# Kernel optimization log

Measured on AMD Instinct MI355X. Metric: run time of the kernel, lower is better.

The kernel has to match this reference:

```python
import jax, jax.numpy as jnp
import numpy as np

N_HEADS = 16

def setup_inputs() -> dict:
    key = jax.random.key(0)
    k1, k2, k3 = jax.random.split(key, 3)
    B, L, D = 2, 2048, 1024
    x = jax.random.normal(k1, (B, L, D), dtype=jnp.float32)
    w_qkv = jax.random.normal(k2, (D, 3 * D), dtype=jnp.float32) * (D ** -0.5)
    w_proj = jax.random.normal(k3, (D, D), dtype=jnp.float32) * (D ** -0.5)
    return {"x": x, "w_qkv": w_qkv, "w_proj": w_proj}

def reference(x, w_qkv, w_proj):
    B, L, D = x.shape
    H = N_HEADS
    dh = D // H
    qkv = x @ w_qkv  # [B,L,3D]
    q, k, v = jnp.split(qkv, 3, axis=-1)
    def heads(t):
        return t.reshape(B, L, H, dh).transpose(0, 2, 1, 3)  # [B,H,L,dh]
    q, k, v = heads(q), heads(k), heads(v)
    s = jnp.einsum('bhqd,bhkd->bhqk', q, k) / jnp.sqrt(jnp.float32(dh))
    causal = jnp.tril(jnp.ones((L, L), dtype=bool))
    s = jnp.where(causal[None, None], s, jnp.float32(-jnp.inf))
    w = jax.nn.softmax(s, axis=-1)
    o = jnp.einsum('bhqk,bhkd->bhqd', w, v)  # [B,H,L,dh]
    o = o.transpose(0, 2, 1, 3).reshape(B, L, D)
    return o @ w_proj
```

## Files before the change

### kernel.cpp

```cpp
#include <hip/hip_runtime.h>
#include <hip/hip_bf16.h>
#include <cstddef>

typedef __attribute__((ext_vector_type(8))) short bf16x8;
typedef __attribute__((ext_vector_type(4))) float f32x4;
typedef __attribute__((ext_vector_type(4))) unsigned short us4;
typedef __attribute__((ext_vector_type(8))) unsigned short us8;
typedef unsigned short u16;
typedef unsigned int u32;

__device__ __forceinline__ u16 f2bf(float f) {
    unsigned u = __builtin_bit_cast(unsigned, f);
    u += 0x7FFFu + ((u >> 16) & 1u);
    return (u16)(u >> 16);
}
__device__ __forceinline__ float bf2f(u16 h) {
    unsigned u = ((unsigned)h) << 16;
    return __builtin_bit_cast(float, u);
}

__device__ __forceinline__ void gl_lds16(const u16* g, u16* l) {
    __builtin_amdgcn_global_load_lds(
        (const __attribute__((address_space(1))) u32*)g,
        (__attribute__((address_space(3))) u32*)l, 16, 0, 0);
}

__device__ __forceinline__ bf16x8 ldswz(const u16* base, int row, int ck) {
    const u16* p = base + row * 64 + ((ck ^ (row & 7)) << 3);
    return __builtin_bit_cast(bf16x8, *(const us8*)p);
}

__global__ __launch_bounds__(256) void split_rm(const float* __restrict__ in,
                                                u16* __restrict__ hi,
                                                u16* __restrict__ lo, int n4) {
    int i = blockIdx.x * 256 + threadIdx.x;
    const int stride = gridDim.x * 256;
    for (; i < n4; i += stride) {
        f32x4 v = ((const f32x4*)in)[i];
        us4 h, l;
#pragma unroll
        for (int e = 0; e < 4; ++e) {
            u16 hb = f2bf(v[e]);
            h[e] = hb;
            l[e] = f2bf(v[e] - bf2f(hb));
        }
        ((us4*)hi)[i] = h;
        ((us4*)lo)[i] = l;
    }
}

__global__ __launch_bounds__(256) void split_T(const float* __restrict__ in, int inRS,
                                               u16* __restrict__ oh,
                                               u16* __restrict__ ol, int outRS) {
    __shared__ u16 Th[64][68], Tl[64][68];
    const int tid = threadIdx.x;
    const int sr = tid >> 4;
    const int sc = (tid & 15) * 4;
    const size_t r0 = (size_t)blockIdx.y * 64;
    const size_t c0 = (size_t)blockIdx.x * 64;

#pragma unroll
    for (int i = 0; i < 4; ++i) {
        int r = sr + i * 16;
        f32x4 v = *(const f32x4*)(in + (r0 + r) * inRS + c0 + sc);
#pragma unroll
        for (int e = 0; e < 4; ++e) {
            u16 hb = f2bf(v[e]);
            Th[sc + e][r] = hb;
            Tl[sc + e][r] = f2bf(v[e] - bf2f(hb));
        }
    }
    __syncthreads();
#pragma unroll
    for (int i = 0; i < 4; ++i) {
        int r = sr + i * 16;
        *(us4*)&oh[(c0 + r) * outRS + r0 + sc] = *(const us4*)&Th[r][sc];
        *(us4*)&ol[(c0 + r) * outRS + r0 + sc] = *(const us4*)&Tl[r][sc];
    }
}

__global__ __launch_bounds__(256) void gemm_bf(
    const u16* __restrict__ Ah_g, const u16* __restrict__ Al_g,
    const u16* __restrict__ Bh_g, const u16* __restrict__ Bl_g,
    int N, int K, int gy, int mode,
    float* __restrict__ Cf,
    u16* __restrict__ qsh, u16* __restrict__ qsl,
    u16* __restrict__ ksh, u16* __restrict__ ksl,
    float* __restrict__ vtmp) {
    __shared__ u16 Ah[128][40], Al[128][40];
    __shared__ u16 Bh[128][40], Bl[128][40];

    const int tid = threadIdx.x;
    const int nwg = gridDim.x;
    const int swz = (blockIdx.x & 7) * (nwg >> 3) + (blockIdx.x >> 3);
    const int bm = (swz % gy) * 128;
    const int bn = (swz / gy) * 128;

    const int arow0 = tid >> 3;
    const int akc   = (tid & 7) * 4;

    const u16* pAh = Ah_g + (size_t)(bm + arow0) * K + akc;
    const u16* pAl = Al_g + (size_t)(bm + arow0) * K + akc;
    const u16* pBh = Bh_g + (size_t)(bn + arow0) * K + akc;
    const u16* pBl = Bl_g + (size_t)(bn + arow0) * K + akc;

    us4 rah[4], ral[4], rbh[4], rbl[4];
#pragma unroll
    for (int c = 0; c < 4; ++c) {
        const size_t o = (size_t)(32 * c) * K;
        rah[c] = *(const us4*)(pAh + o);
        ral[c] = *(const us4*)(pAl + o);
        rbh[c] = *(const us4*)(pBh + o);
        rbl[c] = *(const us4*)(pBl + o);
    }

    const int lane = tid & 63;
    const int w    = tid >> 6;
    const int wm   = (w >> 1) * 64;
    const int wn   = (w & 1) * 64;
    const int lr   = lane & 15;
    const int lg   = lane >> 4;
    const int kb   = lg * 8;

    f32x4 acc[4][4] = {};

    const int NK = K >> 5;
    for (int kt = 0; kt < NK; ++kt) {
#pragma unroll
        for (int c = 0; c < 4; ++c) {
            const int row = arow0 + c * 32;
            *(us4*)&Ah[row][akc] = rah[c];
            *(us4*)&Al[row][akc] = ral[c];
            *(us4*)&Bh[row][akc] = rbh[c];
            *(us4*)&Bl[row][akc] = rbl[c];
        }
        __syncthreads();

        if (kt + 1 < NK) {
            pAh += 32; pAl += 32; pBh += 32; pBl += 32;
#pragma unroll
            for (int c = 0; c < 4; ++c) {
                const size_t o = (size_t)(32 * c) * K;
                rah[c] = *(const us4*)(pAh + o);
                ral[c] = *(const us4*)(pAl + o);
                rbh[c] = *(const us4*)(pBh + o);
                rbl[c] = *(const us4*)(pBl + o);
            }
        }

        bf16x8 fah[4], fal[4], fbh[4], fbl[4];
#pragma unroll
        for (int m = 0; m < 4; ++m) {
            fah[m] = __builtin_bit_cast(bf16x8, *(const us8*)&Ah[wm + m * 16 + lr][kb]);
            fal[m] = __builtin_bit_cast(bf16x8, *(const us8*)&Al[wm + m * 16 + lr][kb]);
        }
#pragma unroll
        for (int n = 0; n < 4; ++n) {
            fbh[n] = __builtin_bit_cast(bf16x8, *(const us8*)&Bh[wn + n * 16 + lr][kb]);
            fbl[n] = __builtin_bit_cast(bf16x8, *(const us8*)&Bl[wn + n * 16 + lr][kb]);
        }
#pragma unroll
        for (int m = 0; m < 4; ++m)
#pragma unroll
            for (int n = 0; n < 4; ++n) {
                acc[m][n] = __builtin_amdgcn_mfma_f32_16x16x32_bf16(fah[m], fbh[n], acc[m][n], 0, 0, 0);
                acc[m][n] = __builtin_amdgcn_mfma_f32_16x16x32_bf16(fah[m], fbl[n], acc[m][n], 0, 0, 0);
                acc[m][n] = __builtin_amdgcn_mfma_f32_16x16x32_bf16(fal[m], fbh[n], acc[m][n], 0, 0, 0);
            }
        __syncthreads();
    }

    const int orow = bm + wm + lg * 4;
    if (mode == 0) {
        const int ocol = bn + wn + lr;
#pragma unroll
        for (int m = 0; m < 4; ++m)
#pragma unroll
            for (int r = 0; r < 4; ++r) {
                const size_t row = (size_t)(orow + m * 16 + r);
#pragma unroll
                for (int n = 0; n < 4; ++n)
                    Cf[row * N + ocol + n * 16] = acc[m][n][r];
            }
    } else {
        const int sec = bn >> 10;
        const int cbase = (bn & 1023) + wn + lr;
#pragma unroll
        for (int m = 0; m < 4; ++m)
#pragma unroll
            for (int r = 0; r < 4; ++r) {
                const size_t row = (size_t)(orow + m * 16 + r);
#pragma unroll
                for (int n = 0; n < 4; ++n) {
                    float v = acc[m][n][r];
                    const size_t idx = row * 1024 + cbase + n * 16;
                    if (sec == 0) {
                        v *= 0.125f;
                        u16 hb = f2bf(v);
                        qsh[idx] = hb;
                        qsl[idx] = f2bf(v - bf2f(hb));
                    } else if (sec == 1) {
                        u16 hb = f2bf(v);
                        ksh[idx] = hb;
                        ksl[idx] = f2bf(v - bf2f(hb));
                    } else {
                        vtmp[idx] = v;
                    }
                }
            }
    }
}

__global__ __launch_bounds__(512, 4) void attn_v2(
    const u16* __restrict__ qsh, const u16* __restrict__ qsl,
    const u16* __restrict__ ksh, const u16* __restrict__ ksl,
    const u16* __restrict__ vth, const u16* __restrict__ vtl,
    u16* __restrict__ oh, u16* __restrict__ ol) {
    __shared__ u16 KH[4096], KL[4096], VH[4096], VL[4096];
    __shared__ u16 Ph[128][72], Pl[128][72];

    const int tid  = threadIdx.x;
    const int lane = tid & 63;
    const int w    = tid >> 6;
    const int wq0  = w * 16;
    const int lr   = lane & 15;
    const int lg   = lane >> 4;

    const int bid  = blockIdx.x;
    const int half = bid >> 8;
    const int idx  = bid & 255;
    const int bh   = idx & 31;
    const int jj   = idx >> 5;
    const int qt   = half ? jj : (15 - jj);
    const int b    = bh >> 4;
    const int h    = bh & 15;
    const int NT   = 2 * qt + 2;
    const size_t tokb = (size_t)b * 2048;

    const size_t qtok = tokb + (size_t)qt * 128 + wq0 + lr;
    const u16* qph = qsh + qtok * 1024 + h * 64 + lg * 8;
    const u16* qpl = qsl + qtok * 1024 + h * 64 + lg * 8;
    bf16x8 aqh[2], aql[2];
    aqh[0] = __builtin_bit_cast(bf16x8, *(const us8*)qph);
    aqh[1] = __builtin_bit_cast(bf16x8, *(const us8*)(qph + 32));
    aql[0] = __builtin_bit_cast(bf16x8, *(const us8*)qpl);
    aql[1] = __builtin_bit_cast(bf16x8, *(const us8*)(qpl + 32));

    const int rl    = lane >> 3;
    const int rbase = w * 8;
    const int cl    = (lane & 7) ^ rl;
    const u16* kh0 = ksh + (tokb + rbase + rl) * 1024 + h * 64 + cl * 8;
    const u16* kl0 = ksl + (tokb + rbase + rl) * 1024 + h * 64 + cl * 8;
    const u16* vh0 = vth + (size_t)(h * 64 + rbase + rl) * 4096 + tokb + cl * 8;
    const u16* vl0 = vtl + (size_t)(h * 64 + rbase + rl) * 4096 + tokb + cl * 8;
    u16* ldsKH = KH + rbase * 64;
    u16* ldsKL = KL + rbase * 64;
    u16* ldsVH = VH + rbase * 64;
    u16* ldsVL = VL + rbase * 64;

    gl_lds16(kh0, ldsKH);
    gl_lds16(kl0, ldsKL);
    gl_lds16(vh0, ldsVH);
    gl_lds16(vl0, ldsVL);

    float m_i[4], l_i[4];
    f32x4 acc_o[4] = {};
#pragma unroll
    for (int r = 0; r < 4; ++r) { m_i[r] = -1e30f; l_i[r] = 0.f; }

    for (int kt = 0; kt < NT; ++kt) {
        const int koff = kt * 64 - qt * 128;
        const bool active = !(kt == NT - 1 && wq0 < 64);

        asm volatile("s_waitcnt vmcnt(2)" ::: "memory");
        __builtin_amdgcn_s_barrier();

        f32x4 accs[4] = {};
        if (active) {
#pragma unroll
            for (int ks = 0; ks < 2; ++ks) {
                bf16x8 a0 = aqh[ks], a1 = aql[ks];
#pragma unroll
                for (int n = 0; n < 4; ++n) {
                    bf16x8 bkh = ldswz(KH, n * 16 + lr, ks * 4 + lg);
                    bf16x8 bkl = ldswz(KL, n * 16 + lr, ks * 4 + lg);
                    accs[n] = __builtin_amdgcn_mfma_f32_16x16x32_bf16(a0, bkh, accs[n], 0, 0, 0);
                    accs[n] = __builtin_amdgcn_mfma_f32_16x16x32_bf16(a0, bkl, accs[n], 0, 0, 0);
                    accs[n] = __builtin_amdgcn_mfma_f32_16x16x32_bf16(a1, bkh, accs[n], 0, 0, 0);
                }
            }
            if (koff + 63 > wq0) {
#pragma unroll
                for (int n = 0; n < 4; ++n)
#pragma unroll
                    for (int rr = 0; rr < 4; ++rr)
                        if (koff + n * 16 + lr > wq0 + 4 * lg + rr)
                            accs[n][rr] = -1e30f;
            }
#pragma unroll
            for (int rr = 0; rr < 4; ++rr) {
                float pm = fmaxf(fmaxf(accs[0][rr], accs[1][rr]),
                                 fmaxf(accs[2][rr], accs[3][rr]));
#pragma unroll
                for (int off = 1; off < 16; off <<= 1)
                    pm = fmaxf(pm, __shfl_xor(pm, off));
                float mnew  = fmaxf(m_i[rr], pm);
                float alpha = __expf(m_i[rr] - mnew);
                float ps = 0.f;
                const int prow = wq0 + 4 * lg + rr;
#pragma unroll
                for (int n = 0; n < 4; ++n) {
                    float p = __expf(accs[n][rr] - mnew);
                    u16 phb = f2bf(p);
                    Ph[prow][n * 16 + lr] = phb;
                    Pl[prow][n * 16 + lr] = f2bf(p - bf2f(phb));
                    ps += p;
                }
#pragma unroll
                for (int off = 1; off < 16; off <<= 1)
                    ps += __shfl_xor(ps, off);
                l_i[rr] = l_i[rr] * alpha + ps;
                m_i[rr] = mnew;
#pragma unroll
                for (int n = 0; n < 4; ++n) acc_o[n][rr] *= alpha;
            }
        }

        asm volatile("s_waitcnt vmcnt(0)" ::: "memory");
        asm volatile("s_waitcnt lgkmcnt(0)" ::: "memory");
        __builtin_amdgcn_s_barrier();

        if (kt + 1 < NT) {
            gl_lds16(kh0 + (size_t)(kt + 1) * 65536, ldsKH);
            gl_lds16(kl0 + (size_t)(kt + 1) * 65536, ldsKL);
        }

        if (active) {
#pragma unroll
            for (int ks = 0; ks < 2; ++ks) {
                bf16x8 aph = __builtin_bit_cast(bf16x8, *(const us8*)&Ph[wq0 + lr][ks * 32 + lg * 8]);
                bf16x8 apl = __builtin_bit_cast(bf16x8, *(const us8*)&Pl[wq0 + lr][ks * 32 + lg * 8]);
#pragma unroll
                for (int n = 0; n < 4; ++n) {
                    bf16x8 bvh = ldswz(VH, n * 16 + lr, ks * 4 + lg);
                    bf16x8 bvl = ldswz(VL, n * 16 + lr, ks * 4 + lg);
                    acc_o[n] = __builtin_amdgcn_mfma_f32_16x16x32_bf16(aph, bvh, acc_o[n], 0, 0, 0);
                    acc_o[n] = __builtin_amdgcn_mfma_f32_16x16x32_bf16(aph, bvl, acc_o[n], 0, 0, 0);
                    acc_o[n] = __builtin_amdgcn_mfma_f32_16x16x32_bf16(apl, bvh, acc_o[n], 0, 0, 0);
                }
            }
        }

        asm volatile("s_waitcnt lgkmcnt(0)" ::: "memory");
        __builtin_amdgcn_s_barrier();

        if (kt + 1 < NT) {
            gl_lds16(vh0 + (kt + 1) * 64, ldsVH);
            gl_lds16(vl0 + (kt + 1) * 64, ldsVL);
        }
    }

#pragma unroll
    for (int rr = 0; rr < 4; ++rr) {
        float inv = 1.0f / l_i[rr];
        const size_t q = (size_t)qt * 128 + wq0 + 4 * lg + rr;
#pragma unroll
        for (int n = 0; n < 4; ++n) {
            float v = acc_o[n][rr] * inv;
            const size_t oidx = (tokb + q) * 1024 + h * 64 + n * 16 + lr;
            u16 hb = f2bf(v);
            oh[oidx] = hb;
            ol[oidx] = f2bf(v - bf2f(hb));
        }
    }
}

extern "C" void kernel_launch(void* const* d_in, const int* in_sizes, int n_in,
                              void* d_out, int out_size, void* d_ws, size_t ws_size,
                              hipStream_t stream) {
    const float* x      = (const float*)d_in[0];
    const float* w_qkv  = (const float*)d_in[1];
    const float* w_proj = (const float*)d_in[2];
    float* out = (float*)d_out;

    char* ws = (char*)d_ws;
    const size_t MB = 1u << 20;
    u16* wqkvT_h  = (u16*)(ws + 0 * MB);
    u16* wqkvT_l  = (u16*)(ws + 6 * MB);
    u16* wprojT_h = (u16*)(ws + 12 * MB);
    u16* wprojT_l = (u16*)(ws + 14 * MB);
    u16* xh       = (u16*)(ws + 16 * MB);
    u16* xl       = (u16*)(ws + 24 * MB);
    u16* qsh      = (u16*)(ws + 32 * MB);
    u16* qsl      = (u16*)(ws + 40 * MB);
    u16* ksh      = (u16*)(ws + 48 * MB);
    u16* ksl      = (u16*)(ws + 56 * MB);
    float* vtmp   = (float*)(ws + 64 * MB);
    u16* vth = xh;
    u16* vtl = xl;
    u16* oh = (u16*)vtmp;
    u16* ol = oh + (size_t)4096 * 1024;

    split_rm<<<2048, 256, 0, stream>>>(x, xh, xl, 4096 * 1024 / 4);
    split_T<<<dim3(48, 16), 256, 0, stream>>>(w_qkv, 3072, wqkvT_h, wqkvT_l, 1024);
    split_T<<<dim3(16, 16), 256, 0, stream>>>(w_proj, 1024, wprojT_h, wprojT_l, 1024);

    gemm_bf<<<dim3(768), 256, 0, stream>>>(xh, xl, wqkvT_h, wqkvT_l,
                                           3072, 1024, 32, 1,
                                           nullptr, qsh, qsl, ksh, ksl, vtmp);

    split_T<<<dim3(16, 64), 256, 0, stream>>>(vtmp, 1024, vth, vtl, 4096);

    attn_v2<<<dim3(512), 512, 0, stream>>>(qsh, qsl, ksh, ksl, vth, vtl, oh, ol);

    gemm_bf<<<dim3(256), 256, 0, stream>>>(oh, ol, wprojT_h, wprojT_l,
                                           1024, 1024, 32, 0,
                                           out, nullptr, nullptr, nullptr, nullptr, nullptr);
}
```

Before: 328.3 us.

## Double-buffer GEMM with direct global-to-LDS loads and swizzled layout

Rewrites the split-bf16 GEMM to stage A/B tiles straight into LDS via global_load_lds, double-buffered with a vmcnt-based wait so the next k-tile loads while MFMAs run. The LDS layout uses an XOR swizzle instead of padding, and the kernel is templated on BN so the output projection uses 128x64 tiles with 512 workgroups for better CU fill. The attention kernel's K/V fragment loads now derive the lo-half address from the hi pointer by a fixed offset. Correctness depends on the hand-counted vmcnt values and on the swizzle matching the load mapping.

```diff
diff --git a/kernel.cpp b/kernel.cpp
--- a/kernel.cpp
+++ b/kernel.cpp
@@ -25,9 +25,11 @@
         (__attribute__((address_space(3))) u32*)l, 16, 0, 0);
 }
 
-__device__ __forceinline__ bf16x8 ldswz(const u16* base, int row, int ck) {
-    const u16* p = base + row * 64 + ((ck ^ (row & 7)) << 3);
-    return __builtin_bit_cast(bf16x8, *(const us8*)p);
+template <int N>
+__device__ __forceinline__ void wait_vmcnt() {
+    if constexpr (N == 8)      asm volatile("s_waitcnt vmcnt(8)" ::: "memory");
+    else if constexpr (N == 6) asm volatile("s_waitcnt vmcnt(6)" ::: "memory");
+    else                       asm volatile("s_waitcnt vmcnt(0)" ::: "memory");
 }
 
 __global__ __launch_bounds__(256) void split_rm(const float* __restrict__ in,
@@ -79,7 +81,8 @@
     }
 }
 
-__global__ __launch_bounds__(256) void gemm_bf(
+template <int BN>
+__global__ __launch_bounds__(256, 2) void gemm_bf2(
     const u16* __restrict__ Ah_g, const u16* __restrict__ Al_g,
     const u16* __restrict__ Bh_g, const u16* __restrict__ Bl_g,
     int N, int K, int gy, int mode,
@@ -87,87 +90,101 @@
     u16* __restrict__ qsh, u16* __restrict__ qsl,
     u16* __restrict__ ksh, u16* __restrict__ ksl,
     float* __restrict__ vtmp) {
-    __shared__ u16 Ah[128][40], Al[128][40];
-    __shared__ u16 Bh[128][40], Bl[128][40];
-
-    const int tid = threadIdx.x;
+    constexpr int NB    = BN / 32;
+    constexpr int ASZ   = 128 * 32;
+    constexpr int BSZ   = BN * 32;
+    constexpr int SET   = 2 * ASZ + 2 * BSZ;
+    constexpr int BCALL = BN / 64;
+    constexpr int NCALL = 4 + 2 * BCALL;
+    __shared__ u16 LB[2 * SET];
+
+    const int tid  = threadIdx.x;
+    const int lane = tid & 63;
+    const int w    = tid >> 6;
+
     const int nwg = gridDim.x;
     const int swz = (blockIdx.x & 7) * (nwg >> 3) + (blockIdx.x >> 3);
     const int bm = (swz % gy) * 128;
-    const int bn = (swz / gy) * 128;
-
-    const int arow0 = tid >> 3;
-    const int akc   = (tid & 7) * 4;
-
-    const u16* pAh = Ah_g + (size_t)(bm + arow0) * K + akc;
-    const u16* pAl = Al_g + (size_t)(bm + arow0) * K + akc;
-    const u16* pBh = Bh_g + (size_t)(bn + arow0) * K + akc;
-    const u16* pBl = Bl_g + (size_t)(bn + arow0) * K + akc;
-
-    us4 rah[4], ral[4], rbh[4], rbl[4];
-#pragma unroll
-    for (int c = 0; c < 4; ++c) {
-        const size_t o = (size_t)(32 * c) * K;
-        rah[c] = *(const us4*)(pAh + o);
-        ral[c] = *(const us4*)(pAl + o);
-        rbh[c] = *(const us4*)(pBh + o);
-        rbl[c] = *(const us4*)(pBl + o);
-    }
-
-    const int lane = tid & 63;
-    const int w    = tid >> 6;
-    const int wm   = (w >> 1) * 64;
-    const int wn   = (w & 1) * 64;
-    const int lr   = lane & 15;
-    const int lg   = lane >> 4;
-    const int kb   = lg * 8;
-
-    f32x4 acc[4][4] = {};
+    const int bn = (swz / gy) * BN;
+
+    const int srow = lane >> 2;
+    const int c_l  = (lane & 3) ^ ((lane >> 3) & 3);
+
+    const u16* pA[2][2];
+    const u16* pB[2][BCALL];
+#pragma unroll
+    for (int j = 0; j < 2; ++j) {
+        const size_t r = (size_t)(bm + w * 32 + j * 16 + srow);
+        pA[0][j] = Ah_g + r * K + c_l * 8;
+        pA[1][j] = Al_g + r * K + c_l * 8;
+    }
+#pragma unroll
+    for (int j = 0; j < BCALL; ++j) {
+        const size_t r = (size_t)(bn + w * (BN / 4) + j * 16 + srow);
+        pB[0][j] = Bh_g + r * K + c_l * 8;
+        pB[1][j] = Bl_g + r * K + c_l * 8;
+    }
+
+    auto stage = [&](int buf, int kt) {
+        u16* s = LB + buf * SET;
+        const size_t ko = (size_t)kt * 32;
+#pragma unroll
+        for (int p = 0; p < 2; ++p)
+#pragma unroll
+            for (int j = 0; j < 2; ++j)
+                gl_lds16(pA[p][j] + ko, s + p * ASZ + (w * 32 + j * 16) * 32);
+#pragma unroll
+        for (int p = 0; p < 2; ++p)
+#pragma unroll
+            for (int j = 0; j < BCALL; ++j)
+                gl_lds16(pB[p][j] + ko,
+                         s + 2 * ASZ + p * BSZ + (w * (BN / 4) + j * 16) * 32);
+    };
+
+    const int lr = lane & 15;
+    const int lg = lane >> 4;
+    const int wm = (w >> 1) * 64;
+    const int wn = (w & 1) * (BN / 2);
+    const int fc = (lg ^ ((lr >> 1) & 3)) * 8;
+
+    f32x4 acc[4][NB] = {};
 
     const int NK = K >> 5;
+    stage(0, 0);
+    if (NK > 1) stage(1, 1);
+
     for (int kt = 0; kt < NK; ++kt) {
-#pragma unroll
-        for (int c = 0; c < 4; ++c) {
-            const int row = arow0 + c * 32;
-            *(us4*)&Ah[row][akc] = rah[c];
-            *(us4*)&Al[row][akc] = ral[c];
-            *(us4*)&Bh[row][akc] = rbh[c];
-            *(us4*)&Bl[row][akc] = rbl[c];
-        }
-        __syncthreads();
-
-        if (kt + 1 < NK) {
-            pAh += 32; pAl += 32; pBh += 32; pBl += 32;
-#pragma unroll
-            for (int c = 0; c < 4; ++c) {
-                const size_t o = (size_t)(32 * c) * K;
-                rah[c] = *(const us4*)(pAh + o);
-                ral[c] = *(const us4*)(pAl + o);
-                rbh[c] = *(const us4*)(pBh + o);
-                rbl[c] = *(const us4*)(pBl + o);
-            }
-        }
-
-        bf16x8 fah[4], fal[4], fbh[4], fbl[4];
+        const int cur = kt & 1;
+        if (kt + 1 < NK) wait_vmcnt<NCALL>();
+        else             wait_vmcnt<0>();
+        __builtin_amdgcn_s_barrier();
+
+        const u16* s = LB + cur * SET;
+        bf16x8 fah[4], fal[4], fbh[NB], fbl[NB];
 #pragma unroll
         for (int m = 0; m < 4; ++m) {
-            fah[m] = __builtin_bit_cast(bf16x8, *(const us8*)&Ah[wm + m * 16 + lr][kb]);
-            fal[m] = __builtin_bit_cast(bf16x8, *(const us8*)&Al[wm + m * 16 + lr][kb]);
-        }
-#pragma unroll
-        for (int n = 0; n < 4; ++n) {
-            fbh[n] = __builtin_bit_cast(bf16x8, *(const us8*)&Bh[wn + n * 16 + lr][kb]);
-            fbl[n] = __builtin_bit_cast(bf16x8, *(const us8*)&Bl[wn + n * 16 + lr][kb]);
+            const int ro = (wm + m * 16 + lr) * 32 + fc;
+            fah[m] = __builtin_bit_cast(bf16x8, *(const us8*)(s + ro));
+            fal[m] = __builtin_bit_cast(bf16x8, *(const us8*)(s + ASZ + ro));
+        }
+#pragma unroll
+        for (int n = 0; n < NB; ++n) {
+            const int ro = (wn + n * 16 + lr) * 32 + fc;
+            fbh[n] = __builtin_bit_cast(bf16x8, *(const us8*)(s + 2 * ASZ + ro));
+            fbl[n] = __builtin_bit_cast(bf16x8, *(const us8*)(s + 2 * ASZ + BSZ + ro));
         }
 #pragma unroll
         for (int m = 0; m < 4; ++m)
 #pragma unroll
-            for (int n = 0; n < 4; ++n) {
+            for (int n = 0; n < NB; ++n) {
                 acc[m][n] = __builtin_amdgcn_mfma_f32_16x16x32_bf16(fah[m], fbh[n], acc[m][n], 0, 0, 0);
                 acc[m][n] = __builtin_amdgcn_mfma_f32_16x16x32_bf16(fah[m], fbl[n], acc[m][n], 0, 0, 0);
                 acc[m][n] = __builtin_amdgcn_mfma_f32_16x16x32_bf16(fal[m], fbh[n], acc[m][n], 0, 0, 0);
             }
-        __syncthreads();
+
+        asm volatile("s_waitcnt lgkmcnt(0)" ::: "memory");
+        __builtin_amdgcn_s_barrier();
+        if (kt + 2 < NK) stage(cur, kt + 2);
     }
 
     const int orow = bm + wm + lg * 4;
@@ -179,7 +196,7 @@
             for (int r = 0; r < 4; ++r) {
                 const size_t row = (size_t)(orow + m * 16 + r);
 #pragma unroll
-                for (int n = 0; n < 4; ++n)
+                for (int n = 0; n < NB; ++n)
                     Cf[row * N + ocol + n * 16] = acc[m][n][r];
             }
     } else {
@@ -191,7 +208,7 @@
             for (int r = 0; r < 4; ++r) {
                 const size_t row = (size_t)(orow + m * 16 + r);
 #pragma unroll
-                for (int n = 0; n < 4; ++n) {
+                for (int n = 0; n < NB; ++n) {
                     float v = acc[m][n][r];
                     const size_t idx = row * 1024 + cbase + n * 16;
                     if (sec == 0) {
@@ -282,8 +299,10 @@
                 bf16x8 a0 = aqh[ks], a1 = aql[ks];
 #pragma unroll
                 for (int n = 0; n < 4; ++n) {
-                    bf16x8 bkh = ldswz(KH, n * 16 + lr, ks * 4 + lg);
-                    bf16x8 bkl = ldswz(KL, n * 16 + lr, ks * 4 + lg);
+                    const int row = n * 16 + lr;
+                    const u16* pk = KH + row * 64 + (((ks * 4 + lg) ^ (row & 7)) << 3);
+                    bf16x8 bkh = __builtin_bit_cast(bf16x8, *(const us8*)pk);
+                    bf16x8 bkl = __builtin_bit_cast(bf16x8, *(const us8*)(pk + 4096));
                     accs[n] = __builtin_amdgcn_mfma_f32_16x16x32_bf16(a0, bkh, accs[n], 0, 0, 0);
                     accs[n] = __builtin_amdgcn_mfma_f32_16x16x32_bf16(a0, bkl, accs[n], 0, 0, 0);
                     accs[n] = __builtin_amdgcn_mfma_f32_16x16x32_bf16(a1, bkh, accs[n], 0, 0, 0);
@@ -342,8 +361,10 @@
                 bf16x8 apl = __builtin_bit_cast(bf16x8, *(const us8*)&Pl[wq0 + lr][ks * 32 + lg * 8]);
 #pragma unroll
                 for (int n = 0; n < 4; ++n) {
-                    bf16x8 bvh = ldswz(VH, n * 16 + lr, ks * 4 + lg);
-                    bf16x8 bvl = ldswz(VL, n * 16 + lr, ks * 4 + lg);
+                    const int row = n * 16 + lr;
+                    const u16* pv = VH + row * 64 + (((ks * 4 + lg) ^ (row & 7)) << 3);
+                    bf16x8 bvh = __builtin_bit_cast(bf16x8, *(const us8*)pv);
+                    bf16x8 bvl = __builtin_bit_cast(bf16x8, *(const us8*)(pv + 4096));
                     acc_o[n] = __builtin_amdgcn_mfma_f32_16x16x32_bf16(aph, bvh, acc_o[n], 0, 0, 0);
                     acc_o[n] = __builtin_amdgcn_mfma_f32_16x16x32_bf16(aph, bvl, acc_o[n], 0, 0, 0);
                     acc_o[n] = __builtin_amdgcn_mfma_f32_16x16x32_bf16(apl, bvh, acc_o[n], 0, 0, 0);
@@ -405,15 +426,15 @@
     split_T<<<dim3(48, 16), 256, 0, stream>>>(w_qkv, 3072, wqkvT_h, wqkvT_l, 1024);
     split_T<<<dim3(16, 16), 256, 0, stream>>>(w_proj, 1024, wprojT_h, wprojT_l, 1024);
 
-    gemm_bf<<<dim3(768), 256, 0, stream>>>(xh, xl, wqkvT_h, wqkvT_l,
-                                           3072, 1024, 32, 1,
-                                           nullptr, qsh, qsl, ksh, ksl, vtmp);
+    gemm_bf2<128><<<dim3(768), 256, 0, stream>>>(xh, xl, wqkvT_h, wqkvT_l,
+                                                 3072, 1024, 32, 1,
+                                                 nullptr, qsh, qsl, ksh, ksl, vtmp);
 
     split_T<<<dim3(16, 64), 256, 0, stream>>>(vtmp, 1024, vth, vtl, 4096);
 
     attn_v2<<<dim3(512), 512, 0, stream>>>(qsh, qsl, ksh, ksl, vth, vtl, oh, ol);
 
-    gemm_bf<<<dim3(256), 256, 0, stream>>>(oh, ol, wprojT_h, wprojT_l,
-                                           1024, 1024, 32, 0,
-                                           out, nullptr, nullptr, nullptr, nullptr, nullptr);
-}
+    gemm_bf2<64><<<dim3(512), 256, 0, stream>>>(oh, ol, wprojT_h, wprojT_l,
+                                                1024, 1024, 32, 0,
+                                                out, nullptr, nullptr, nullptr, nullptr, nullptr);
+}
```

Result: no change. 322.6 us (-1.8%).
